# Performance work log

Measured on AMD Instinct MI355X. Metric: run time of the kernel, lower is better.

## Reference

```python
import jax, jax.numpy as jnp
import numpy as np

TEMPERATURE = 0.5
EPS = 1e-12  # matches torch F.normalize clamp_min


def setup_inputs() -> dict:
    key = jax.random.key(0)
    k1, k2 = jax.random.split(key)
    N, D, C = 8192, 128, 64
    out_1 = jax.random.normal(k1, (N, D), dtype=jnp.float32)
    label = jax.random.randint(k2, (N,), 0, C, dtype=jnp.int64)
    return {"out_1": out_1, "label": label}


def reference(out_1, label):
    N = out_1.shape[0]
    # L2 normalize rows (F.normalize with eps clamp)
    norm = jnp.maximum(jnp.linalg.norm(out_1, axis=-1, keepdims=True), EPS)
    x = out_1 / norm
    # exp-scaled cosine similarity matrix [N, N]
    sim = jnp.exp(jnp.matmul(x, x.T) / TEMPERATURE)
    not_diag = 1.0 - jnp.eye(N, dtype=sim.dtype)
    # negatives: all off-diagonal entries per row
    negative_sim = jnp.sum(sim * not_diag, axis=-1)
    # positives: same label, excluding self; mean per row
    pos_mask = (label[:, None] == label[None, :]).astype(sim.dtype) * not_diag
    pos_count = jnp.sum(pos_mask, axis=-1)
    pos_sim = jnp.sum(sim * pos_mask, axis=-1) / pos_count
    return jnp.mean(-jnp.log(pos_sim / negative_sim))
```

## Files before the change

kernel.cpp:

```cpp
#include <hip/hip_runtime.h>
#include <hip/hip_bf16.h>
#include <stdint.h>

typedef __attribute__((ext_vector_type(8))) __bf16 bf16x8;
typedef __attribute__((ext_vector_type(16))) float floatx16;

#if __has_builtin(__builtin_amdgcn_exp2f)
#define EXP2F(x) __builtin_amdgcn_exp2f(x)
#else
#define EXP2F(x) exp2f(x)
#endif

#define GAS __attribute__((address_space(1)))
#define LAS __attribute__((address_space(3)))

#define SCALE_SQRT 1.69864359f
#define JCH 8

__global__ __launch_bounds__(256) void k_prep(const float* __restrict__ x,
                                              const int* __restrict__ raw,
                                              ushort* __restrict__ xb,
                                              int* __restrict__ lab, int N) {
  const int row = (blockIdx.x * 256 + threadIdx.x) >> 6;
  const int lane = threadIdx.x & 63;
  if (row >= N) return;
  const int probe = raw[2 * lane + 1];
  const bool is64 = (__ballot(probe != 0) == 0ull);
  const float2 v = ((const float2*)(x + (size_t)row * 128))[lane];
  float ss = v.x * v.x + v.y * v.y;
#pragma unroll
  for (int m = 1; m < 64; m <<= 1) ss += __shfl_xor(ss, m, 64);
  const float rn = SCALE_SQRT / fmaxf(sqrtf(ss), 1e-12f);
  __hip_bfloat162 o;
  o.x = __float2bfloat16(v.x * rn);
  o.y = __float2bfloat16(v.y * rn);
  ((__hip_bfloat162*)xb)[row * 64 + lane] = o;
  if (lane == 0) lab[row] = is64 ? raw[2 * row] : raw[row];
}

__global__ __launch_bounds__(256, 2) void k_sim(const ushort* __restrict__ xb,
                                                const int* __restrict__ lab,
                                                float* __restrict__ pneg,
                                                float* __restrict__ ppos,
                                                int N, int jpb) {
  __shared__ ushort ldsA[128 * 128];
  __shared__ ushort ldsB[2][64 * 128];
  const int tid = threadIdx.x;
  const int lane = tid & 63;
  const int wv = tid >> 6;
  const int wy = wv >> 1, wx = wv & 1;
  const int l31 = lane & 31, g2 = lane >> 5;
  const int l15 = lane & 15, g4 = lane >> 4;
  const int i0 = blockIdx.y * 128;
  const int c = blockIdx.x;
  const int jt0 = c * jpb;

  auto rowOff = [&](int t) -> int {
    const int reg = t & 15, mi = t >> 4;
    return wy * 64 + mi * 32 + (reg & 3) + 8 * (reg >> 2) + 4 * g2;
  };

#pragma unroll
  for (int it = 0; it < 8; ++it) {
    const int r0 = it * 16 + wv * 4;
    const int lr = r0 + g4;
    const int kb = l15 ^ (lr & 15);
    const ushort* gp = xb + (size_t)(i0 + lr) * 128 + kb * 8;
    __builtin_amdgcn_global_load_lds((GAS void*)gp, (LAS void*)&ldsA[r0 * 128], 16, 0, 0);
  }
  {
    const int j0 = jt0 * 64;
#pragma unroll
    for (int it = 0; it < 4; ++it) {
      const int r0 = it * 16 + wv * 4;
      const int lr = r0 + g4;
      const int kb = l15 ^ (lr & 15);
      const ushort* gp = xb + (size_t)(j0 + lr) * 128 + kb * 8;
      __builtin_amdgcn_global_load_lds((GAS void*)gp, (LAS void*)&ldsB[0][r0 * 128], 16, 0, 0);
    }
  }

  int li[32];
  float neg[32], pos[32];
#pragma unroll
  for (int t = 0; t < 32; ++t) {
    li[t] = lab[i0 + rowOff(t)];
    neg[t] = 0.0f;
    pos[t] = 0.0f;
  }
  __syncthreads();

  for (int t = 0; t < jpb; ++t) {
    const int j0 = (jt0 + t) * 64;
    const int buf = t & 1;
    if (t + 1 < jpb) {
      const int jn = j0 + 64;
#pragma unroll
      for (int it = 0; it < 4; ++it) {
        const int r0 = it * 16 + wv * 4;
        const int lr = r0 + g4;
        const int kb = l15 ^ (lr & 15);
        const ushort* gp = xb + (size_t)(jn + lr) * 128 + kb * 8;
        __builtin_amdgcn_global_load_lds((GAS void*)gp, (LAS void*)&ldsB[buf ^ 1][r0 * 128], 16, 0, 0);
      }
    }
    const int lj = lab[j0 + wx * 32 + l31];

    floatx16 acc[2];
    acc[0] = (floatx16)(0.0f);
    acc[1] = (floatx16)(0.0f);
#pragma unroll
    for (int kt = 0; kt < 8; ++kt) {
      const int brow = wx * 32 + l31;
      const int bkb = (kt * 2 + g2) ^ (brow & 15);
      const bf16x8 bfr = *(const bf16x8*)&ldsB[buf][brow * 128 + bkb * 8];
#pragma unroll
      for (int mi = 0; mi < 2; ++mi) {
        const int arow = wy * 64 + mi * 32 + l31;
        const int akb = (kt * 2 + g2) ^ (arow & 15);
        const bf16x8 af = *(const bf16x8*)&ldsA[arow * 128 + akb * 8];
        acc[mi] = __builtin_amdgcn_mfma_f32_32x32x16_bf16(af, bfr, acc[mi], 0, 0, 0);
      }
    }

    const int dlt = j0 - i0;
    const bool diag = ((unsigned)dlt < 128u);
    const int jc = wx * 32 + l31 + dlt;
    auto epi = [&](bool DG) {
#pragma unroll
      for (int mi = 0; mi < 2; ++mi) {
#pragma unroll
        for (int reg = 0; reg < 16; ++reg) {
          float e = EXP2F(acc[mi][reg]);
          if (DG) {
            const int ir = wy * 64 + mi * 32 + (reg & 3) + 8 * (reg >> 2) + 4 * g2;
            if (ir == jc) e = 0.0f;
          }
          neg[mi * 16 + reg] += e;
          pos[mi * 16 + reg] += (li[mi * 16 + reg] == lj) ? e : 0.0f;
        }
      }
    };
    if (diag) epi(true); else epi(false);
    __syncthreads();
  }

  float* fl = (float*)ldsB;
#pragma unroll
  for (int t = 0; t < 32; ++t) {
    float n = neg[t], p = pos[t];
#pragma unroll
    for (int m = 1; m < 32; m <<= 1) {
      n += __shfl_xor(n, m, 64);
      p += __shfl_xor(p, m, 64);
    }
    if (l31 == 0) {
      const int r = rowOff(t);
      fl[(r * 2 + 0) * 2 + wx] = n;
      fl[(r * 2 + 1) * 2 + wx] = p;
    }
  }
  __syncthreads();
  if (tid < 128) {
    const int r = tid;
    pneg[(size_t)c * N + i0 + r] = fl[(r * 2 + 0) * 2] + fl[(r * 2 + 0) * 2 + 1];
    ppos[(size_t)c * N + i0 + r] = fl[(r * 2 + 1) * 2] + fl[(r * 2 + 1) * 2 + 1];
  }
}

__global__ __launch_bounds__(1024) void k_final(const float* __restrict__ pneg,
                                                const float* __restrict__ ppos,
                                                const int* __restrict__ lab,
                                                float* __restrict__ out, int N) {
  __shared__ int h[64];
  if (threadIdx.x < 64) h[threadIdx.x] = 0;
  __syncthreads();
  for (int i = threadIdx.x; i < N; i += 1024) atomicAdd(&h[lab[i] & 63], 1);
  __syncthreads();
  double s = 0.0;
  for (int i = threadIdx.x; i < N; i += 1024) {
    float n = 0.0f, p = 0.0f;
#pragma unroll
    for (int c = 0; c < JCH; ++c) {
      n += pneg[(size_t)c * N + i];
      p += ppos[(size_t)c * N + i];
    }
    const float cnt = (float)(h[lab[i] & 63] - 1);
    s += (double)logf(n * cnt / p);
  }
#pragma unroll
  for (int m = 1; m < 64; m <<= 1) s += __shfl_xor(s, m, 64);
  __shared__ double wsum[16];
  if ((threadIdx.x & 63) == 0) wsum[threadIdx.x >> 6] = s;
  __syncthreads();
  if (threadIdx.x == 0) {
    double tot = 0.0;
    for (int w = 0; w < 16; ++w) tot += wsum[w];
    out[0] = (float)(tot / (double)N);
  }
}

extern "C" void kernel_launch(void* const* d_in, const int* in_sizes, int n_in,
                              void* d_out, int out_size, void* d_ws, size_t ws_size,
                              hipStream_t stream) {
  const float* x = (const float*)d_in[0];
  const int* raw_label = (const int*)d_in[1];
  const int N = in_sizes[1];
  char* ws = (char*)d_ws;
  ushort* xb = (ushort*)ws;
  float* pneg = (float*)(ws + (size_t)N * 128 * 2);
  float* ppos = pneg + (size_t)JCH * N;
  int* lab = (int*)(ppos + (size_t)JCH * N);
  float* out = (float*)d_out;

  const int jpb = (N / 64) / JCH;

  k_prep<<<dim3(N / 4), dim3(256), 0, stream>>>(x, raw_label, xb, lab, N);
  k_sim<<<dim3(JCH, N / 128), dim3(256), 0, stream>>>(xb, lab, pneg, ppos, N, jpb);
  k_final<<<dim3(1), dim3(1024), 0, stream>>>(pneg, ppos, lab, out, N);
}
```

Baseline: 101.8 us.

## Keep A fragments in registers, remap waves to rows, parallelize final reduction

The similarity kernel no longer stages the 128-row A tile in LDS. Each wave now owns 32 rows and loads its A fragments straight into registers, then multiplies them against the full 64-column B tile. This removes A's LDS traffic, cuts LDS use (which may allow more occupancy), and drops the cross-wave LDS reduction at the end. It also adds s_setprio around the MFMA loop, and splits the single-block final reduction into a multi-block pass plus a tiny write kernel. The trade-offs are more registers for the A fragments and one extra kernel launch; each block also rebuilds the label histogram redundantly.

```diff
diff --git a/kernel.cpp b/kernel.cpp
--- a/kernel.cpp
+++ b/kernel.cpp
@@ -43,31 +43,16 @@
                                                 float* __restrict__ pneg,
                                                 float* __restrict__ ppos,
                                                 int N, int jpb) {
-  __shared__ ushort ldsA[128 * 128];
   __shared__ ushort ldsB[2][64 * 128];
   const int tid = threadIdx.x;
   const int lane = tid & 63;
   const int wv = tid >> 6;
-  const int wy = wv >> 1, wx = wv & 1;
   const int l31 = lane & 31, g2 = lane >> 5;
   const int l15 = lane & 15, g4 = lane >> 4;
   const int i0 = blockIdx.y * 128;
   const int c = blockIdx.x;
   const int jt0 = c * jpb;
 
-  auto rowOff = [&](int t) -> int {
-    const int reg = t & 15, mi = t >> 4;
-    return wy * 64 + mi * 32 + (reg & 3) + 8 * (reg >> 2) + 4 * g2;
-  };
-
-#pragma unroll
-  for (int it = 0; it < 8; ++it) {
-    const int r0 = it * 16 + wv * 4;
-    const int lr = r0 + g4;
-    const int kb = l15 ^ (lr & 15);
-    const ushort* gp = xb + (size_t)(i0 + lr) * 128 + kb * 8;
-    __builtin_amdgcn_global_load_lds((GAS void*)gp, (LAS void*)&ldsA[r0 * 128], 16, 0, 0);
-  }
   {
     const int j0 = jt0 * 64;
 #pragma unroll
@@ -80,13 +65,19 @@
     }
   }
 
-  int li[32];
-  float neg[32], pos[32];
-#pragma unroll
-  for (int t = 0; t < 32; ++t) {
-    li[t] = lab[i0 + rowOff(t)];
-    neg[t] = 0.0f;
-    pos[t] = 0.0f;
+  const int arow = i0 + wv * 32 + l31;
+  bf16x8 af[8];
+#pragma unroll
+  for (int kt = 0; kt < 8; ++kt)
+    af[kt] = *(const bf16x8*)(xb + (size_t)arow * 128 + (kt * 2 + g2) * 8);
+
+  int li[16];
+  float neg[16], pos[16];
+#pragma unroll
+  for (int r = 0; r < 16; ++r) {
+    li[r] = lab[i0 + wv * 32 + (r & 3) + 8 * (r >> 2) + 4 * g2];
+    neg[r] = 0.0f;
+    pos[r] = 0.0f;
   }
   __syncthreads();
 
@@ -104,40 +95,41 @@
         __builtin_amdgcn_global_load_lds((GAS void*)gp, (LAS void*)&ldsB[buf ^ 1][r0 * 128], 16, 0, 0);
       }
     }
-    const int lj = lab[j0 + wx * 32 + l31];
+    const int lj0 = lab[j0 + l31];
+    const int lj1 = lab[j0 + 32 + l31];
 
     floatx16 acc[2];
     acc[0] = (floatx16)(0.0f);
     acc[1] = (floatx16)(0.0f);
+    __builtin_amdgcn_s_setprio(1);
 #pragma unroll
     for (int kt = 0; kt < 8; ++kt) {
-      const int brow = wx * 32 + l31;
-      const int bkb = (kt * 2 + g2) ^ (brow & 15);
-      const bf16x8 bfr = *(const bf16x8*)&ldsB[buf][brow * 128 + bkb * 8];
-#pragma unroll
-      for (int mi = 0; mi < 2; ++mi) {
-        const int arow = wy * 64 + mi * 32 + l31;
-        const int akb = (kt * 2 + g2) ^ (arow & 15);
-        const bf16x8 af = *(const bf16x8*)&ldsA[arow * 128 + akb * 8];
-        acc[mi] = __builtin_amdgcn_mfma_f32_32x32x16_bf16(af, bfr, acc[mi], 0, 0, 0);
+#pragma unroll
+      for (int h = 0; h < 2; ++h) {
+        const int brow = h * 32 + l31;
+        const int bkb = (kt * 2 + g2) ^ (brow & 15);
+        const bf16x8 bfr = *(const bf16x8*)&ldsB[buf][brow * 128 + bkb * 8];
+        acc[h] = __builtin_amdgcn_mfma_f32_32x32x16_bf16(af[kt], bfr, acc[h], 0, 0, 0);
       }
     }
+    __builtin_amdgcn_s_setprio(0);
 
     const int dlt = j0 - i0;
     const bool diag = ((unsigned)dlt < 128u);
-    const int jc = wx * 32 + l31 + dlt;
     auto epi = [&](bool DG) {
 #pragma unroll
-      for (int mi = 0; mi < 2; ++mi) {
-#pragma unroll
-        for (int reg = 0; reg < 16; ++reg) {
-          float e = EXP2F(acc[mi][reg]);
+      for (int h = 0; h < 2; ++h) {
+        const int lj = h ? lj1 : lj0;
+        const int jc = h * 32 + l31 + dlt;
+#pragma unroll
+        for (int r = 0; r < 16; ++r) {
+          float e = EXP2F(acc[h][r]);
           if (DG) {
-            const int ir = wy * 64 + mi * 32 + (reg & 3) + 8 * (reg >> 2) + 4 * g2;
+            const int ir = wv * 32 + (r & 3) + 8 * (r >> 2) + 4 * g2;
             if (ir == jc) e = 0.0f;
           }
-          neg[mi * 16 + reg] += e;
-          pos[mi * 16 + reg] += (li[mi * 16 + reg] == lj) ? e : 0.0f;
+          neg[r] += e;
+          pos[r] += (li[r] == lj) ? e : 0.0f;
         }
       }
     };
@@ -145,59 +137,60 @@
     __syncthreads();
   }
 
-  float* fl = (float*)ldsB;
-#pragma unroll
-  for (int t = 0; t < 32; ++t) {
-    float n = neg[t], p = pos[t];
+#pragma unroll
+  for (int r = 0; r < 16; ++r) {
+    float n = neg[r], p = pos[r];
 #pragma unroll
     for (int m = 1; m < 32; m <<= 1) {
       n += __shfl_xor(n, m, 64);
       p += __shfl_xor(p, m, 64);
     }
     if (l31 == 0) {
-      const int r = rowOff(t);
-      fl[(r * 2 + 0) * 2 + wx] = n;
-      fl[(r * 2 + 1) * 2 + wx] = p;
-    }
-  }
-  __syncthreads();
-  if (tid < 128) {
-    const int r = tid;
-    pneg[(size_t)c * N + i0 + r] = fl[(r * 2 + 0) * 2] + fl[(r * 2 + 0) * 2 + 1];
-    ppos[(size_t)c * N + i0 + r] = fl[(r * 2 + 1) * 2] + fl[(r * 2 + 1) * 2 + 1];
-  }
-}
-
-__global__ __launch_bounds__(1024) void k_final(const float* __restrict__ pneg,
-                                                const float* __restrict__ ppos,
-                                                const int* __restrict__ lab,
-                                                float* __restrict__ out, int N) {
+      const int row = i0 + wv * 32 + (r & 3) + 8 * (r >> 2) + 4 * g2;
+      pneg[(size_t)c * N + row] = n;
+      ppos[(size_t)c * N + row] = p;
+    }
+  }
+}
+
+__global__ __launch_bounds__(256) void k_final(const float* __restrict__ pneg,
+                                               const float* __restrict__ ppos,
+                                               const int* __restrict__ lab,
+                                               double* __restrict__ partial, int N) {
   __shared__ int h[64];
-  if (threadIdx.x < 64) h[threadIdx.x] = 0;
-  __syncthreads();
-  for (int i = threadIdx.x; i < N; i += 1024) atomicAdd(&h[lab[i] & 63], 1);
-  __syncthreads();
-  double s = 0.0;
-  for (int i = threadIdx.x; i < N; i += 1024) {
+  __shared__ double wsum[4];
+  const int tid = threadIdx.x;
+  if (tid < 64) h[tid] = 0;
+  __syncthreads();
+  for (int i = tid; i < N; i += 256) atomicAdd(&h[lab[i] & 63], 1);
+  __syncthreads();
+  const int r = blockIdx.x * 256 + tid;
+  double v = 0.0;
+  if (r < N) {
     float n = 0.0f, p = 0.0f;
 #pragma unroll
-    for (int c = 0; c < JCH; ++c) {
-      n += pneg[(size_t)c * N + i];
-      p += ppos[(size_t)c * N + i];
-    }
-    const float cnt = (float)(h[lab[i] & 63] - 1);
-    s += (double)logf(n * cnt / p);
-  }
-#pragma unroll
-  for (int m = 1; m < 64; m <<= 1) s += __shfl_xor(s, m, 64);
-  __shared__ double wsum[16];
-  if ((threadIdx.x & 63) == 0) wsum[threadIdx.x >> 6] = s;
-  __syncthreads();
-  if (threadIdx.x == 0) {
-    double tot = 0.0;
-    for (int w = 0; w < 16; ++w) tot += wsum[w];
-    out[0] = (float)(tot / (double)N);
-  }
+    for (int cc = 0; cc < JCH; ++cc) {
+      n += pneg[(size_t)cc * N + r];
+      p += ppos[(size_t)cc * N + r];
+    }
+    const float cnt = (float)(h[lab[r] & 63] - 1);
+    v = (double)logf(n * cnt / p);
+  }
+#pragma unroll
+  for (int m = 1; m < 64; m <<= 1) v += __shfl_xor(v, m, 64);
+  if ((tid & 63) == 0) wsum[tid >> 6] = v;
+  __syncthreads();
+  if (tid == 0) partial[blockIdx.x] = wsum[0] + wsum[1] + wsum[2] + wsum[3];
+}
+
+__global__ __launch_bounds__(64) void k_write(const double* __restrict__ partial,
+                                              float* __restrict__ out, int nfb, int N) {
+  const int l = threadIdx.x;
+  double v = 0.0;
+  for (int i = l; i < nfb; i += 64) v += partial[i];
+#pragma unroll
+  for (int m = 1; m < 64; m <<= 1) v += __shfl_xor(v, m, 64);
+  if (l == 0) out[0] = (float)(v / (double)N);
 }
 
 extern "C" void kernel_launch(void* const* d_in, const int* in_sizes, int n_in,
@@ -211,11 +204,14 @@
   float* pneg = (float*)(ws + (size_t)N * 128 * 2);
   float* ppos = pneg + (size_t)JCH * N;
   int* lab = (int*)(ppos + (size_t)JCH * N);
+  double* partial = (double*)(lab + N);
   float* out = (float*)d_out;
 
   const int jpb = (N / 64) / JCH;
+  const int nfb = (N + 255) / 256;
 
   k_prep<<<dim3(N / 4), dim3(256), 0, stream>>>(x, raw_label, xb, lab, N);
   k_sim<<<dim3(JCH, N / 128), dim3(256), 0, stream>>>(xb, lab, pneg, ppos, N, jpb);
-  k_final<<<dim3(1), dim3(1024), 0, stream>>>(pneg, ppos, lab, out, N);
-}
+  k_final<<<dim3(nfb), dim3(256), 0, stream>>>(pneg, ppos, lab, partial, N);
+  k_write<<<dim3(1), dim3(64), 0, stream>>>(partial, out, nfb, N);
+}
```

After: 98.06 us. 1.04x faster.
